# Kernel optimization log

Measured on AMD Instinct MI355X. Metric: run time of the kernel, lower is better.

## Reference

```python
import jax, jax.numpy as jnp
import numpy as np
from jax import lax

EPS = 1e-6


def setup_inputs() -> dict:
    key = jax.random.key(0)
    k1, k2, k3, k4 = jax.random.split(key, 4)
    B, M, N = 256, 256, 256
    A_re = jax.random.normal(k1, (B, M, N), dtype=jnp.float32)
    A_im = jax.random.normal(k2, (B, M, N), dtype=jnp.float32)
    v_re = jax.random.uniform(k3, (B, N, 1), dtype=jnp.float32)
    v_im = jax.random.uniform(k4, (B, N, 1), dtype=jnp.float32)
    return {"A_re": A_re, "A_im": A_im, "v_re": v_re, "v_im": v_im, "num_iter": 30}


def reference(A_re, A_im, v_re, v_im, num_iter):
    A = (A_re + 1j * A_im).astype(jnp.complex64)          # [B, M, N]
    v = (v_re + 1j * v_im).astype(jnp.complex64)          # [B, N, 1]
    # AhA = A^H A : [B, N, N]
    AhA = jnp.einsum('bmn,bmk->bnk', jnp.conj(A), A)

    def step(v, _):
        v = jnp.matmul(AhA, v)                            # [B, N, 1]
        # ||v||_2 over the N axis -> [B, 1]
        eig = jnp.sqrt(jnp.sum(v.real**2 + v.imag**2, axis=1))
        v = v / (eig[:, :, None] + EPS)
        return v, eig

    v, eigs = lax.scan(step, v, None, length=num_iter)
    return eigs[-1].reshape(-1)                           # [B]
```

## Files before the change

kernel.cpp:

```cpp
#include <hip/hip_runtime.h>
#include <cstdint>

typedef _Float16 f16;
typedef _Float16 f16x2 __attribute__((ext_vector_type(2)));
typedef _Float16 f16x8 __attribute__((ext_vector_type(8)));
typedef float    f32x4 __attribute__((ext_vector_type(4)));

static __device__ __forceinline__ uint32_t pack2(float x, float y) {
    f16 hx = (f16)x, hy = (f16)y;
    uint32_t ux = __builtin_bit_cast(unsigned short, hx);
    uint32_t uy = __builtin_bit_cast(unsigned short, hy);
    return ux | (uy << 16);
}

static __device__ __forceinline__ void lds_barrier() {
    __builtin_amdgcn_sched_barrier(0);
    asm volatile("s_waitcnt lgkmcnt(0)");
    __builtin_amdgcn_s_barrier();
    __builtin_amdgcn_sched_barrier(0);
}

__global__ __launch_bounds__(512, 2) void k_gemm(const float* __restrict__ Are,
                                                 const float* __restrict__ Aim,
                                                 f16* __restrict__ AhAre,
                                                 f16* __restrict__ AhAim) {
    const int tid = threadIdx.x;
    const int b = blockIdx.x;

    __shared__ __align__(16) f16 ls[2][2][256 * 32];

    const int l = tid & 63, g = tid >> 6;
    const int lr = l & 15, lk = l >> 4;

    const int u = tid & 15;
    const int fp = tid >> 4;
    const int su = u >> 2, uq = u & 3;

    f16* oR = AhAre + (size_t)b * 65536;
    f16* oI = AhAim + (size_t)b * 65536;

    {
        f32x4 cR[16], cI[16];
#pragma unroll
        for (int j = 0; j < 16; ++j) { cR[j] = (f32x4)0.0f; cI[j] = (f32x4)0.0f; }

        float4 v[2][4];
#pragma unroll
        for (int t = 0; t < 2; ++t) {
            const float* sp = (t ? Aim : Are) + (size_t)b * 65536
                            + (size_t)(2 * u) * 256 + fp * 8;
            v[t][0] = *(const float4*)(sp);
            v[t][1] = *(const float4*)(sp + 4);
            v[t][2] = *(const float4*)(sp + 256);
            v[t][3] = *(const float4*)(sp + 260);
        }

#pragma unroll
        for (int step = 0; step < 8; ++step) {
            const int p = step & 1;

#pragma unroll
            for (int t = 0; t < 2; ++t) {
                float xv[8] = {v[t][0].x, v[t][0].y, v[t][0].z, v[t][0].w,
                               v[t][1].x, v[t][1].y, v[t][1].z, v[t][1].w};
                float yv[8] = {v[t][2].x, v[t][2].y, v[t][2].z, v[t][2].w,
                               v[t][3].x, v[t][3].y, v[t][3].z, v[t][3].w};
                uint32_t* lw = (uint32_t*)&ls[p][t][0];
#pragma unroll
                for (int i = 0; i < 8; ++i) {
                    int r = fp * 8 + i;
                    int s = su ^ ((r >> 1) & 3);
                    lw[r * 16 + s * 4 + uq] = pack2(xv[i], yv[i]);
                }
            }

            if (step < 7) {
                const int m0n = 32 * (step + 1);
#pragma unroll
                for (int t = 0; t < 2; ++t) {
                    const float* sp = (t ? Aim : Are) + (size_t)b * 65536
                                    + (size_t)(m0n + 2 * u) * 256 + fp * 8;
                    v[t][0] = *(const float4*)(sp);
                    v[t][1] = *(const float4*)(sp + 4);
                    v[t][2] = *(const float4*)(sp + 256);
                    v[t][3] = *(const float4*)(sp + 260);
                }
            }

            lds_barrier();

            const f16* lsR = &ls[p][0][0];
            const f16* lsI = &ls[p][1][0];

            const int r1 = 16 * g + lr;
            const int s1 = lk ^ ((r1 >> 1) & 3);
            f16x8 a1re = *(const f16x8*)(&lsR[r1 * 32 + s1 * 8]);
            uint4 u1   = *(const uint4*)(&lsI[r1 * 32 + s1 * 8]);
            f16x8 a1im = __builtin_bit_cast(f16x8, u1);
            uint4 n1 = make_uint4(u1.x ^ 0x80008000u, u1.y ^ 0x80008000u,
                                  u1.z ^ 0x80008000u, u1.w ^ 0x80008000u);
            f16x8 na1 = __builtin_bit_cast(f16x8, n1);

#pragma unroll
            for (int j = 0; j < 16; ++j) {
                int rb = 16 * j + lr;
                int sb = lk ^ ((rb >> 1) & 3);
                f16x8 bre = *(const f16x8*)(&lsR[rb * 32 + sb * 8]);
                f16x8 bim = *(const f16x8*)(&lsI[rb * 32 + sb * 8]);
                cR[j] = __builtin_amdgcn_mfma_f32_16x16x32_f16(a1re, bre, cR[j], 0, 0, 0);
                cR[j] = __builtin_amdgcn_mfma_f32_16x16x32_f16(a1im, bim, cR[j], 0, 0, 0);
                cI[j] = __builtin_amdgcn_mfma_f32_16x16x32_f16(a1re, bim, cI[j], 0, 0, 0);
                cI[j] = __builtin_amdgcn_mfma_f32_16x16x32_f16(na1,  bre, cI[j], 0, 0, 0);
            }
        }

#pragma unroll
        for (int j = 0; j < 16; ++j)
#pragma unroll
            for (int r = 0; r < 4; ++r) {
                int n = 16 * g + lk * 4 + r;
                int c = 16 * j + lr;
                oR[(size_t)n * 256 + c] = (f16)cR[j][r];
                oI[(size_t)n * 256 + c] = (f16)cI[j][r];
            }

        f16* lsm = &ls[0][0][0];
        const int jj_out = tid >> 2, qtr = tid & 3;

        __syncthreads();
#pragma unroll
        for (int j = 8; j < 16; ++j)
#pragma unroll
            for (int r = 0; r < 4; ++r) {
                int jj = 16 * (j - 8) + lr;
                int nn = 16 * g + lk * 4 + r;
                lsm[jj * 128 + nn] = (f16)cR[j][r];
            }
        __syncthreads();
        {
            const f16* srow = lsm + jj_out * 128 + qtr * 32;
            f16* drow = oR + (size_t)(128 + jj_out) * 256 + qtr * 32;
#pragma unroll
            for (int ch = 0; ch < 4; ++ch)
                *(uint4*)(void*)(drow + ch * 8) = *(const uint4*)(srow + ch * 8);
        }
        __syncthreads();
#pragma unroll
        for (int j = 8; j < 16; ++j)
#pragma unroll
            for (int r = 0; r < 4; ++r) {
                int jj = 16 * (j - 8) + lr;
                int nn = 16 * g + lk * 4 + r;
                lsm[jj * 128 + nn] = (f16)(-cI[j][r]);
            }
        __syncthreads();
        {
            const f16* srow = lsm + jj_out * 128 + qtr * 32;
            f16* drow = oI + (size_t)(128 + jj_out) * 256 + qtr * 32;
#pragma unroll
            for (int ch = 0; ch < 4; ++ch)
                *(uint4*)(void*)(drow + ch * 8) = *(const uint4*)(srow + ch * 8);
        }
        __syncthreads();
    }

    {
        f32x4 dR[8], dI[8];
#pragma unroll
        for (int j = 0; j < 8; ++j) { dR[j] = (f32x4)0.0f; dI[j] = (f32x4)0.0f; }

        float4 w[2][2];
#pragma unroll
        for (int t = 0; t < 2; ++t) {
            const float* sp = (t ? Aim : Are) + (size_t)b * 65536
                            + (size_t)(2 * u) * 256 + 128 + fp * 4;
            w[t][0] = *(const float4*)(sp);
            w[t][1] = *(const float4*)(sp + 256);
        }

#pragma unroll
        for (int step = 0; step < 8; ++step) {
            const int p = step & 1;

#pragma unroll
            for (int t = 0; t < 2; ++t) {
                float xv[4] = {w[t][0].x, w[t][0].y, w[t][0].z, w[t][0].w};
                float yv[4] = {w[t][1].x, w[t][1].y, w[t][1].z, w[t][1].w};
                uint32_t* lw = (uint32_t*)&ls[p][t][0];
#pragma unroll
                for (int i = 0; i < 4; ++i) {
                    int rr = fp * 4 + i;
                    int s = su ^ ((rr >> 1) & 3);
                    lw[rr * 16 + s * 4 + uq] = pack2(xv[i], yv[i]);
                }
            }

            if (step < 7) {
                const int m0n = 32 * (step + 1);
#pragma unroll
                for (int t = 0; t < 2; ++t) {
                    const float* sp = (t ? Aim : Are) + (size_t)b * 65536
                                    + (size_t)(m0n + 2 * u) * 256 + 128 + fp * 4;
                    w[t][0] = *(const float4*)(sp);
                    w[t][1] = *(const float4*)(sp + 256);
                }
            }

            lds_barrier();

            const f16* lsR = &ls[p][0][0];
            const f16* lsI = &ls[p][1][0];

            const int r2 = 16 * g + lr;
            const int s2 = lk ^ ((r2 >> 1) & 3);
            f16x8 a2re = *(const f16x8*)(&lsR[r2 * 32 + s2 * 8]);
            uint4 u2   = *(const uint4*)(&lsI[r2 * 32 + s2 * 8]);
            f16x8 a2im = __builtin_bit_cast(f16x8, u2);
            uint4 n2 = make_uint4(u2.x ^ 0x80008000u, u2.y ^ 0x80008000u,
                                  u2.z ^ 0x80008000u, u2.w ^ 0x80008000u);
            f16x8 na2 = __builtin_bit_cast(f16x8, n2);

#pragma unroll
            for (int j = 0; j < 8; ++j) {
                int rb = 16 * j + lr;
                int sb = lk ^ ((rb >> 1) & 3);
                f16x8 bre = *(const f16x8*)(&lsR[rb * 32 + sb * 8]);
                f16x8 bim = *(const f16x8*)(&lsI[rb * 32 + sb * 8]);
                dR[j] = __builtin_amdgcn_mfma_f32_16x16x32_f16(a2re, bre, dR[j], 0, 0, 0);
                dR[j] = __builtin_amdgcn_mfma_f32_16x16x32_f16(a2im, bim, dR[j], 0, 0, 0);
                dI[j] = __builtin_amdgcn_mfma_f32_16x16x32_f16(a2re, bim, dI[j], 0, 0, 0);
                dI[j] = __builtin_amdgcn_mfma_f32_16x16x32_f16(na2,  bre, dI[j], 0, 0, 0);
            }
        }

#pragma unroll
        for (int j = 0; j < 8; ++j)
#pragma unroll
            for (int r = 0; r < 4; ++r) {
                int n = 128 + 16 * g + lk * 4 + r;
                int c = 128 + 16 * j + lr;
                oR[(size_t)n * 256 + c] = (f16)dR[j][r];
                oI[(size_t)n * 256 + c] = (f16)dI[j][r];
            }
    }
}

static __device__ __forceinline__ void matvec2(const f16x8 (&afr)[2][16],
                                               const f16* __restrict__ vs, int h,
                                               float4 (&y)[2]) {
    f16x8 bf[16];
#pragma unroll
    for (int c = 0; c < 16; ++c) bf[c] = *(const f16x8*)(vs + 32 * c + 8 * h);
    f32x4 P0[2], P1[2];
#pragma unroll
    for (int rg = 0; rg < 2; ++rg) { P0[rg] = (f32x4)0.0f; P1[rg] = (f32x4)0.0f; }
#pragma unroll
    for (int c = 0; c < 16; ++c) {
#pragma unroll
        for (int rg = 0; rg < 2; ++rg) {
            if (c & 1) P1[rg] = __builtin_amdgcn_mfma_f32_16x16x32_f16(afr[rg][c], bf[c], P1[rg], 0, 0, 0);
            else       P0[rg] = __builtin_amdgcn_mfma_f32_16x16x32_f16(afr[rg][c], bf[c], P0[rg], 0, 0, 0);
        }
    }
#pragma unroll
    for (int rg = 0; rg < 2; ++rg)
        y[rg] = make_float4(P0[rg][0] + P1[rg][0], P0[rg][1] + P1[rg][1],
                            P0[rg][2] + P1[rg][2], P0[rg][3] + P1[rg][3]);
}

__global__ __launch_bounds__(512, 2) void k_power(const f16* __restrict__ AhAre,
                                                  const f16* __restrict__ AhAim,
                                                  const float* __restrict__ vre,
                                                  const float* __restrict__ vim,
                                                  const int* __restrict__ pniter,
                                                  float* __restrict__ out) {
    const int tid = threadIdx.x;
    const int b = blockIdx.x;
    const int l = tid & 63;
    const int g = tid >> 6;
    const int sel = l & 15;
    const int h = l >> 4;

    __shared__ __align__(16) f16 v0h[2][512];
    __shared__ __align__(16) f16 v1h[2][512];
    __shared__ __align__(16) float part[2][8];

    f16x8 afr[2][16];
#pragma unroll
    for (int rg = 0; rg < 2; ++rg) {
        const int m = 32 * g + 16 * rg + sel;
        const f16* bR = AhAre + (size_t)b * 65536 + (size_t)m * 256 + 8 * h;
        const f16* bI = AhAim + (size_t)b * 65536 + (size_t)m * 256 + 8 * h;
#pragma unroll
        for (int c = 0; c < 8; ++c) {
            afr[rg][c]     = *(const f16x8*)(bR + 32 * c);
            afr[rg][8 + c] = *(const f16x8*)(bI + 32 * c);
        }
    }
#pragma unroll
    for (int rg = 0; rg < 2; ++rg)
#pragma unroll
        for (int c = 0; c < 16; ++c) asm volatile("" : "+a"(afr[rg][c]));

    if (tid < 256) {
        float xr = vre[b * 256 + tid], xi = vim[b * 256 + tid];
        v0h[0][tid]       = (f16)xr;
        v0h[0][256 + tid] = (f16)(-xi);
        v1h[0][tid]       = (f16)xi;
        v1h[0][256 + tid] = (f16)xr;
    }
    __syncthreads();

    const int niter = *pniter;
    const f16* vsel = (sel == 0) ? &v0h[0][0] : &v1h[0][0];

    float eig = 0.0f;

    auto npart = [&](int wb, const float4 (&y)[2]) {
        float s_ = 0.0f;
        if (sel < 2) {
#pragma unroll
            for (int rg = 0; rg < 2; ++rg)
                s_ += y[rg].x * y[rg].x + y[rg].y * y[rg].y
                    + y[rg].z * y[rg].z + y[rg].w * y[rg].w;
        }
        s_ += __shfl_xor(s_, 1, 64);
        s_ += __shfl_xor(s_, 16, 64);
        s_ += __shfl_xor(s_, 32, 64);
        if (l == 0) part[wb][g] = s_;
    };
    auto vwrite = [&](int wb, const float4 (&y)[2], float sc) {
        if (sel < 2) {
#pragma unroll
            for (int rg = 0; rg < 2; ++rg) {
                uint32_t w0 = pack2(y[rg].x * sc, y[rg].y * sc);
                uint32_t w1 = pack2(y[rg].z * sc, y[rg].w * sc);
                int m0 = 32 * g + 16 * rg + 4 * h;
                if (sel == 0) {
                    *(uint2*)(void*)(&v0h[wb][m0])       = make_uint2(w0, w1);
                    *(uint2*)(void*)(&v1h[wb][256 + m0]) = make_uint2(w0, w1);
                } else {
                    *(uint2*)(void*)(&v1h[wb][m0])       = make_uint2(w0, w1);
                    *(uint2*)(void*)(&v0h[wb][256 + m0]) =
                        make_uint2(w0 ^ 0x80008000u, w1 ^ 0x80008000u);
                }
            }
        }
    };
    auto psum = [&](int rb) -> float {
        float4 q0 = *(const float4*)(&part[rb][0]);
        float4 q1 = *(const float4*)(&part[rb][4]);
        return (q0.x + q0.y + q0.z + q0.w) + (q1.x + q1.y + q1.z + q1.w);
    };

    float sc_m1 = 1.0f;
    float nm2   = 1.0f;

    float4 y[2];

    if (niter >= 1) {
        matvec2(afr, vsel, h, y);
        npart(1, y);
        __syncthreads();
        float e1v = sqrtf(psum(1));
        float sc  = __builtin_amdgcn_rcpf(e1v + 1e-6f);
        vwrite(1, y, sc);
        eig = e1v;
        __syncthreads();
    }
    if (niter >= 2) {
        matvec2(afr, vsel + 512, h, y);
        npart(0, y);
        __syncthreads();
        float e2v = sqrtf(psum(0));
        float sc  = __builtin_amdgcn_rcpf(e2v + 1e-6f);
        vwrite(0, y, sc);
        eig = e2v;
        sc_m1 = sc;
        nm2   = 1.0f;
        __syncthreads();
    }

    int wr = 0;
    for (int t = 3; t <= niter; ++t) {
        const int rd = wr;
        wr ^= 1;
        float q   = psum(rd);
        float e1v = __builtin_amdgcn_sqrtf(q);
        float nm1 = e1v * sc_m1;
        float sc  = nm2 * __builtin_amdgcn_rcpf(e1v * nm1 + 1e-12f);
        matvec2(afr, vsel + (size_t)rd * 512, h, y);
        vwrite(wr, y, sc);
        npart(wr, y);
        nm2 = nm1; sc_m1 = sc;
        __syncthreads();
    }

    if (niter >= 3) {
        float qT = psum(wr);
        eig = sqrtf(qT) / (nm2 + 1e-12f);
    }
    if (tid == 0) out[b] = eig;
}

extern "C" void kernel_launch(void* const* d_in, const int* in_sizes, int n_in,
                              void* d_out, int out_size, void* d_ws, size_t ws_size,
                              hipStream_t stream) {
    const float* Are = (const float*)d_in[0];
    const float* Aim = (const float*)d_in[1];
    const float* vre = (const float*)d_in[2];
    const float* vim = (const float*)d_in[3];
    const int* niter = (const int*)d_in[4];
    float* out = (float*)d_out;

    f16* AhAre = (f16*)d_ws;
    f16* AhAim = (f16*)((char*)d_ws + (size_t)32 * 1024 * 1024);

    k_gemm<<<dim3(256), dim3(512), 0, stream>>>(Are, Aim, AhAre, AhAim);
    k_power<<<dim3(256), dim3(512), 0, stream>>>(AhAre, AhAim, vre, vim, niter, out);
}
```

Measured before the change: 101.9 us.

## Double Gram GEMM block to 1024 threads, splitting columns across wave groups

The A^H A kernel now launches 1024 threads per batch instead of 512. The 16 waves form an 8x2 grid, and each wave computes half the column tiles it computed before, so it holds half the accumulators and does half the staging loads. This is meant to raise per-block wave parallelism and cut per-thread work and register pressure, since there are only 256 blocks on a large GPU. In exchange the block is larger, and fewer blocks may fit per CU while barriers cover more waves.

```diff
diff --git a/kernel.cpp b/kernel.cpp
--- a/kernel.cpp
+++ b/kernel.cpp
@@ -2,7 +2,6 @@
 #include <cstdint>
 
 typedef _Float16 f16;
-typedef _Float16 f16x2 __attribute__((ext_vector_type(2)));
 typedef _Float16 f16x8 __attribute__((ext_vector_type(8)));
 typedef float    f32x4 __attribute__((ext_vector_type(4)));
 
@@ -20,16 +19,17 @@
     __builtin_amdgcn_sched_barrier(0);
 }
 
-__global__ __launch_bounds__(512, 2) void k_gemm(const float* __restrict__ Are,
-                                                 const float* __restrict__ Aim,
-                                                 f16* __restrict__ AhAre,
-                                                 f16* __restrict__ AhAim) {
+__global__ __launch_bounds__(1024) void k_gemm(const float* __restrict__ Are,
+                                               const float* __restrict__ Aim,
+                                               f16* __restrict__ AhAre,
+                                               f16* __restrict__ AhAim) {
     const int tid = threadIdx.x;
     const int b = blockIdx.x;
 
     __shared__ __align__(16) f16 ls[2][2][256 * 32];
 
     const int l = tid & 63, g = tid >> 6;
+    const int gr = g & 7, gc = g >> 3;
     const int lr = l & 15, lk = l >> 4;
 
     const int u = tid & 15;
@@ -40,19 +40,17 @@
     f16* oI = AhAim + (size_t)b * 65536;
 
     {
-        f32x4 cR[16], cI[16];
-#pragma unroll
-        for (int j = 0; j < 16; ++j) { cR[j] = (f32x4)0.0f; cI[j] = (f32x4)0.0f; }
-
-        float4 v[2][4];
+        f32x4 cR[8], cI[8];
+#pragma unroll
+        for (int j = 0; j < 8; ++j) { cR[j] = (f32x4)0.0f; cI[j] = (f32x4)0.0f; }
+
+        float4 v[2][2];
 #pragma unroll
         for (int t = 0; t < 2; ++t) {
             const float* sp = (t ? Aim : Are) + (size_t)b * 65536
-                            + (size_t)(2 * u) * 256 + fp * 8;
+                            + (size_t)(2 * u) * 256 + fp * 4;
             v[t][0] = *(const float4*)(sp);
-            v[t][1] = *(const float4*)(sp + 4);
-            v[t][2] = *(const float4*)(sp + 256);
-            v[t][3] = *(const float4*)(sp + 260);
+            v[t][1] = *(const float4*)(sp + 256);
         }
 
 #pragma unroll
@@ -61,14 +59,12 @@
 
 #pragma unroll
             for (int t = 0; t < 2; ++t) {
-                float xv[8] = {v[t][0].x, v[t][0].y, v[t][0].z, v[t][0].w,
-                               v[t][1].x, v[t][1].y, v[t][1].z, v[t][1].w};
-                float yv[8] = {v[t][2].x, v[t][2].y, v[t][2].z, v[t][2].w,
-                               v[t][3].x, v[t][3].y, v[t][3].z, v[t][3].w};
+                float xv[4] = {v[t][0].x, v[t][0].y, v[t][0].z, v[t][0].w};
+                float yv[4] = {v[t][1].x, v[t][1].y, v[t][1].z, v[t][1].w};
                 uint32_t* lw = (uint32_t*)&ls[p][t][0];
 #pragma unroll
-                for (int i = 0; i < 8; ++i) {
-                    int r = fp * 8 + i;
+                for (int i = 0; i < 4; ++i) {
+                    int r = fp * 4 + i;
                     int s = su ^ ((r >> 1) & 3);
                     lw[r * 16 + s * 4 + uq] = pack2(xv[i], yv[i]);
                 }
@@ -79,11 +75,9 @@
 #pragma unroll
                 for (int t = 0; t < 2; ++t) {
                     const float* sp = (t ? Aim : Are) + (size_t)b * 65536
-                                    + (size_t)(m0n + 2 * u) * 256 + fp * 8;
+                                    + (size_t)(m0n + 2 * u) * 256 + fp * 4;
                     v[t][0] = *(const float4*)(sp);
-                    v[t][1] = *(const float4*)(sp + 4);
-                    v[t][2] = *(const float4*)(sp + 256);
-                    v[t][3] = *(const float4*)(sp + 260);
+                    v[t][1] = *(const float4*)(sp + 256);
                 }
             }
 
@@ -92,7 +86,7 @@
             const f16* lsR = &ls[p][0][0];
             const f16* lsI = &ls[p][1][0];
 
-            const int r1 = 16 * g + lr;
+            const int r1 = 16 * gr + lr;
             const int s1 = lk ^ ((r1 >> 1) & 3);
             f16x8 a1re = *(const f16x8*)(&lsR[r1 * 32 + s1 * 8]);
             uint4 u1   = *(const uint4*)(&lsI[r1 * 32 + s1 * 8]);
@@ -102,8 +96,8 @@
             f16x8 na1 = __builtin_bit_cast(f16x8, n1);
 
 #pragma unroll
-            for (int j = 0; j < 16; ++j) {
-                int rb = 16 * j + lr;
+            for (int j = 0; j < 8; ++j) {
+                int rb = 128 * gc + 16 * j + lr;
                 int sb = lk ^ ((rb >> 1) & 3);
                 f16x8 bre = *(const f16x8*)(&lsR[rb * 32 + sb * 8]);
                 f16x8 bim = *(const f16x8*)(&lsI[rb * 32 + sb * 8]);
@@ -115,67 +109,69 @@
         }
 
 #pragma unroll
-        for (int j = 0; j < 16; ++j)
+        for (int j = 0; j < 8; ++j)
 #pragma unroll
             for (int r = 0; r < 4; ++r) {
-                int n = 16 * g + lk * 4 + r;
-                int c = 16 * j + lr;
+                int n = 16 * gr + lk * 4 + r;
+                int c = 128 * gc + 16 * j + lr;
                 oR[(size_t)n * 256 + c] = (f16)cR[j][r];
                 oI[(size_t)n * 256 + c] = (f16)cI[j][r];
             }
 
         f16* lsm = &ls[0][0][0];
-        const int jj_out = tid >> 2, qtr = tid & 3;
-
-        __syncthreads();
-#pragma unroll
-        for (int j = 8; j < 16; ++j)
-#pragma unroll
-            for (int r = 0; r < 4; ++r) {
-                int jj = 16 * (j - 8) + lr;
-                int nn = 16 * g + lk * 4 + r;
-                lsm[jj * 128 + nn] = (f16)cR[j][r];
-            }
+        const int jjo = tid >> 3, q8 = tid & 7;
+
+        __syncthreads();
+        if (gc == 1) {
+#pragma unroll
+            for (int j = 0; j < 8; ++j)
+#pragma unroll
+                for (int r = 0; r < 4; ++r) {
+                    int jj = 16 * j + lr;
+                    int nn = 16 * gr + lk * 4 + r;
+                    lsm[jj * 128 + nn] = (f16)cR[j][r];
+                }
+        }
         __syncthreads();
         {
-            const f16* srow = lsm + jj_out * 128 + qtr * 32;
-            f16* drow = oR + (size_t)(128 + jj_out) * 256 + qtr * 32;
-#pragma unroll
-            for (int ch = 0; ch < 4; ++ch)
-                *(uint4*)(void*)(drow + ch * 8) = *(const uint4*)(srow + ch * 8);
-        }
-        __syncthreads();
-#pragma unroll
-        for (int j = 8; j < 16; ++j)
-#pragma unroll
-            for (int r = 0; r < 4; ++r) {
-                int jj = 16 * (j - 8) + lr;
-                int nn = 16 * g + lk * 4 + r;
-                lsm[jj * 128 + nn] = (f16)(-cI[j][r]);
-            }
+            const f16* srow = lsm + jjo * 128 + q8 * 16;
+            f16* drow = oR + (size_t)(128 + jjo) * 256 + q8 * 16;
+            *(uint4*)(void*)(drow)     = *(const uint4*)(srow);
+            *(uint4*)(void*)(drow + 8) = *(const uint4*)(srow + 8);
+        }
+        __syncthreads();
+        if (gc == 1) {
+#pragma unroll
+            for (int j = 0; j < 8; ++j)
+#pragma unroll
+                for (int r = 0; r < 4; ++r) {
+                    int jj = 16 * j + lr;
+                    int nn = 16 * gr + lk * 4 + r;
+                    lsm[jj * 128 + nn] = (f16)(-cI[j][r]);
+                }
+        }
         __syncthreads();
         {
-            const f16* srow = lsm + jj_out * 128 + qtr * 32;
-            f16* drow = oI + (size_t)(128 + jj_out) * 256 + qtr * 32;
-#pragma unroll
-            for (int ch = 0; ch < 4; ++ch)
-                *(uint4*)(void*)(drow + ch * 8) = *(const uint4*)(srow + ch * 8);
+            const f16* srow = lsm + jjo * 128 + q8 * 16;
+            f16* drow = oI + (size_t)(128 + jjo) * 256 + q8 * 16;
+            *(uint4*)(void*)(drow)     = *(const uint4*)(srow);
+            *(uint4*)(void*)(drow + 8) = *(const uint4*)(srow + 8);
         }
         __syncthreads();
     }
 
     {
-        f32x4 dR[8], dI[8];
-#pragma unroll
-        for (int j = 0; j < 8; ++j) { dR[j] = (f32x4)0.0f; dI[j] = (f32x4)0.0f; }
-
-        float4 w[2][2];
+        f32x4 dR[4], dI[4];
+#pragma unroll
+        for (int j = 0; j < 4; ++j) { dR[j] = (f32x4)0.0f; dI[j] = (f32x4)0.0f; }
+
+        float2 w[2][2];
 #pragma unroll
         for (int t = 0; t < 2; ++t) {
             const float* sp = (t ? Aim : Are) + (size_t)b * 65536
-                            + (size_t)(2 * u) * 256 + 128 + fp * 4;
-            w[t][0] = *(const float4*)(sp);
-            w[t][1] = *(const float4*)(sp + 256);
+                            + (size_t)(2 * u) * 256 + 128 + fp * 2;
+            w[t][0] = *(const float2*)(sp);
+            w[t][1] = *(const float2*)(sp + 256);
         }
 
 #pragma unroll
@@ -184,14 +180,14 @@
 
 #pragma unroll
             for (int t = 0; t < 2; ++t) {
-                float xv[4] = {w[t][0].x, w[t][0].y, w[t][0].z, w[t][0].w};
-                float yv[4] = {w[t][1].x, w[t][1].y, w[t][1].z, w[t][1].w};
+                float xv[2] = {w[t][0].x, w[t][0].y};
+                float yv[2] = {w[t][1].x, w[t][1].y};
                 uint32_t* lw = (uint32_t*)&ls[p][t][0];
 #pragma unroll
-                for (int i = 0; i < 4; ++i) {
-                    int rr = fp * 4 + i;
-                    int s = su ^ ((rr >> 1) & 3);
-                    lw[rr * 16 + s * 4 + uq] = pack2(xv[i], yv[i]);
+                for (int i = 0; i < 2; ++i) {
+                    int r = fp * 2 + i;
+                    int s = su ^ ((r >> 1) & 3);
+                    lw[r * 16 + s * 4 + uq] = pack2(xv[i], yv[i]);
                 }
             }
 
@@ -200,9 +196,9 @@
 #pragma unroll
                 for (int t = 0; t < 2; ++t) {
                     const float* sp = (t ? Aim : Are) + (size_t)b * 65536
-                                    + (size_t)(m0n + 2 * u) * 256 + 128 + fp * 4;
-                    w[t][0] = *(const float4*)(sp);
-                    w[t][1] = *(const float4*)(sp + 256);
+                                    + (size_t)(m0n + 2 * u) * 256 + 128 + fp * 2;
+                    w[t][0] = *(const float2*)(sp);
+                    w[t][1] = *(const float2*)(sp + 256);
                 }
             }
 
@@ -211,7 +207,7 @@
             const f16* lsR = &ls[p][0][0];
             const f16* lsI = &ls[p][1][0];
 
-            const int r2 = 16 * g + lr;
+            const int r2 = 16 * gr + lr;
             const int s2 = lk ^ ((r2 >> 1) & 3);
             f16x8 a2re = *(const f16x8*)(&lsR[r2 * 32 + s2 * 8]);
             uint4 u2   = *(const uint4*)(&lsI[r2 * 32 + s2 * 8]);
@@ -221,8 +217,8 @@
             f16x8 na2 = __builtin_bit_cast(f16x8, n2);
 
 #pragma unroll
-            for (int j = 0; j < 8; ++j) {
-                int rb = 16 * j + lr;
+            for (int j = 0; j < 4; ++j) {
+                int rb = 64 * gc + 16 * j + lr;
                 int sb = lk ^ ((rb >> 1) & 3);
                 f16x8 bre = *(const f16x8*)(&lsR[rb * 32 + sb * 8]);
                 f16x8 bim = *(const f16x8*)(&lsI[rb * 32 + sb * 8]);
@@ -234,11 +230,11 @@
         }
 
 #pragma unroll
-        for (int j = 0; j < 8; ++j)
+        for (int j = 0; j < 4; ++j)
 #pragma unroll
             for (int r = 0; r < 4; ++r) {
-                int n = 128 + 16 * g + lk * 4 + r;
-                int c = 128 + 16 * j + lr;
+                int n = 128 + 16 * gr + lk * 4 + r;
+                int c = 128 + 64 * gc + 16 * j + lr;
                 oR[(size_t)n * 256 + c] = (f16)dR[j][r];
                 oI[(size_t)n * 256 + c] = (f16)dI[j][r];
             }
@@ -416,6 +412,6 @@
     f16* AhAre = (f16*)d_ws;
     f16* AhAim = (f16*)((char*)d_ws + (size_t)32 * 1024 * 1024);
 
-    k_gemm<<<dim3(256), dim3(512), 0, stream>>>(Are, Aim, AhAre, AhAim);
+    k_gemm<<<dim3(256), dim3(1024), 0, stream>>>(Are, Aim, AhAre, AhAim);
     k_power<<<dim3(256), dim3(512), 0, stream>>>(AhAre, AhAim, vre, vim, niter, out);
 }
```

Measured after the change: 125.5 us. 1.23x slower.
